# Optimization experiments

Measured on AMD Instinct MI355X. Metric: run time of the kernel, lower is better.

## Reference

```python
import jax, jax.numpy as jnp
import numpy as np

D_MODEL = 1024
N_HEADS = 16
D_K = 64
CHUNK_LEN = 64


def setup_inputs() -> dict:
    key = jax.random.key(0)
    ks = jax.random.split(key, 10)
    B, S = 4, 2048
    NC, NN, NL = 32, 2, 128
    s = 1.0 / np.sqrt(D_MODEL)
    inp = {
        "query": jax.random.normal(ks[0], (B, S, D_MODEL), dtype=jnp.float32),
        "key": jax.random.normal(ks[1], (B, NC, NN, NL, D_MODEL), dtype=jnp.float32),
        # Linear weights stored as [in, out] (equivalent to torch W.T)
        "Wq": jax.random.normal(ks[2], (D_MODEL, N_HEADS * D_K), dtype=jnp.float32) * s,
        "bq": jnp.zeros((N_HEADS * D_K,), dtype=jnp.float32),
        "Wk": jax.random.normal(ks[3], (D_MODEL, N_HEADS * D_K), dtype=jnp.float32) * s,
        "bk": jnp.zeros((N_HEADS * D_K,), dtype=jnp.float32),
        "Wv": jax.random.normal(ks[4], (D_MODEL, N_HEADS * D_K), dtype=jnp.float32) * s,
        "bv": jnp.zeros((N_HEADS * D_K,), dtype=jnp.float32),
        "Wo": jax.random.normal(ks[5], (N_HEADS * D_K, D_MODEL), dtype=jnp.float32) * s,
        "bo": jnp.zeros((D_MODEL,), dtype=jnp.float32),
    }
    return inp


def reference(query, key, Wq, bq, Wk, bk, Wv, bv, Wo, bo):
    B, S, D = query.shape
    _, NC, NN, NL, _ = key.shape
    L = NN * NL  # kv length per chunk
    # reshape query into chunks: [B, NC, chunk_len, D]
    q_in = query.reshape(B, NC, CHUNK_LEN, D)
    kv_in = key.reshape(B, NC, L, D)  # key used for both K and V in the original
    # projections, split heads: [B, NC, H, T, d_k]
    q = (q_in @ Wq + bq).reshape(B, NC, CHUNK_LEN, N_HEADS, D_K).transpose(0, 1, 3, 2, 4)
    k = (kv_in @ Wk + bk).reshape(B, NC, L, N_HEADS, D_K).transpose(0, 1, 3, 2, 4)
    v = (kv_in @ Wv + bv).reshape(B, NC, L, N_HEADS, D_K).transpose(0, 1, 3, 2, 4)
    # attention per (batch, chunk, head)
    scores = jnp.einsum("bchqd,bchkd->bchqk", q, k) / jnp.sqrt(jnp.float32(D_K))
    attn = jax.nn.softmax(scores, axis=-1)
    o = jnp.einsum("bchqk,bchkd->bchqd", attn, v)
    # merge heads: [B, NC, chunk_len, H*d_k]
    o = o.transpose(0, 1, 3, 2, 4).reshape(B, NC, CHUNK_LEN, N_HEADS * D_K)
    out = o @ Wo + bo
    return out.reshape(B, S, D)
```

## Files before the change

### kernel.cpp

```cpp
#include <hip/hip_runtime.h>
#include <hip/hip_bf16.h>
#include <stdint.h>

#define DMODEL 1024
#define NHEADS 16
#define DK 64
#define TQ 64
#define LKV 256
#define MQ 8192
#define MKV 32768

typedef __bf16 bf16x8 __attribute__((ext_vector_type(8)));
typedef float f32x4 __attribute__((ext_vector_type(4)));
typedef unsigned short u16x8 __attribute__((ext_vector_type(8)));

__device__ __forceinline__ unsigned short f2bf(float f) {
    union { float f; unsigned int i; } x; x.f = f;
    unsigned int r = (x.i + 0x7FFFu + ((x.i >> 16) & 1u)) >> 16;
    return (unsigned short)r;
}

__device__ __forceinline__ void gload_lds16(const void* g, void* l) {
    __builtin_amdgcn_global_load_lds(
        (const __attribute__((address_space(1))) unsigned int*)g,
        (__attribute__((address_space(3))) unsigned int*)l, 16, 0, 0);
}

__global__ __launch_bounds__(256) void cvt_f32_bf16(const float* __restrict__ in,
                                                    unsigned short* __restrict__ out) {
    long long i = ((long long)blockIdx.x * 256 + threadIdx.x) * 8;
    f32x4 a = *(const f32x4*)(in + i);
    f32x4 b = *(const f32x4*)(in + i + 4);
    u16x8 o;
    o[0] = f2bf(a[0]); o[1] = f2bf(a[1]); o[2] = f2bf(a[2]); o[3] = f2bf(a[3]);
    o[4] = f2bf(b[0]); o[5] = f2bf(b[1]); o[6] = f2bf(b[2]); o[7] = f2bf(b[3]);
    *(u16x8*)(out + i) = o;
}

__global__ __launch_bounds__(256) void transpose_w_cvt(const float* __restrict__ in,
                                                       unsigned short* __restrict__ out) {
    __shared__ float tile[64][65];
    int bi = blockIdx.y, bj = blockIdx.x;
    int tid = threadIdx.x;
    int c = tid & 63, r0 = tid >> 6;
#pragma unroll
    for (int p = 0; p < 16; ++p) {
        int r = r0 + 4 * p;
        tile[r][c] = in[(size_t)(bi * 64 + r) * 1024 + bj * 64 + c];
    }
    __syncthreads();
#pragma unroll
    for (int p = 0; p < 16; ++p) {
        int r = r0 + 4 * p;
        out[(size_t)(bj * 64 + r) * 1024 + bi * 64 + c] = f2bf(tile[c][r]);
    }
}

template <int OUTMODE>
__global__ __launch_bounds__(256) void gemm_bias(const unsigned short* __restrict__ A,
                                                 const unsigned short* __restrict__ Bt,
                                                 const float* __restrict__ bias,
                                                 void* __restrict__ OutV) {
    __shared__ alignas(16) unsigned short aLds[128 * 32];
    __shared__ alignas(16) unsigned short bLds[128 * 32];

    int tid = threadIdx.x;
    int lane = tid & 63, wid = tid >> 6;
    int m0 = blockIdx.x * 128;
    int n0 = blockIdx.y * 128;
    int wr = (wid >> 1) * 64, wc = (wid & 1) * 64;

    f32x4 zero = {0.f, 0.f, 0.f, 0.f};
    f32x4 acc[4][4];
#pragma unroll
    for (int i = 0; i < 4; ++i)
#pragma unroll
        for (int j = 0; j < 4; ++j) acc[i][j] = zero;

    int sr = lane >> 2;
    int sk = (lane & 3) * 8;
    const unsigned short* aG = A + (size_t)(m0 + sr) * 1024 + sk;
    const unsigned short* bG = Bt + (size_t)(n0 + sr) * 1024 + sk;
    int c0 = wid, c1 = wid + 4;

    int fr = lane & 15, fg = (lane >> 4) * 8;

    for (int kt = 0; kt < 1024; kt += 32) {
        gload_lds16(aG + (size_t)(c0 * 16) * 1024 + kt, aLds + c0 * 512);
        gload_lds16(aG + (size_t)(c1 * 16) * 1024 + kt, aLds + c1 * 512);
        gload_lds16(bG + (size_t)(c0 * 16) * 1024 + kt, bLds + c0 * 512);
        gload_lds16(bG + (size_t)(c1 * 16) * 1024 + kt, bLds + c1 * 512);
        __syncthreads();

        bf16x8 af[4], bf[4];
#pragma unroll
        for (int mt = 0; mt < 4; ++mt)
            af[mt] = *(const bf16x8*)&aLds[(wr + mt * 16 + fr) * 32 + fg];
#pragma unroll
        for (int nt = 0; nt < 4; ++nt)
            bf[nt] = *(const bf16x8*)&bLds[(wc + nt * 16 + fr) * 32 + fg];
#pragma unroll
        for (int mt = 0; mt < 4; ++mt)
#pragma unroll
            for (int nt = 0; nt < 4; ++nt)
                acc[mt][nt] = __builtin_amdgcn_mfma_f32_16x16x32_bf16(af[mt], bf[nt], acc[mt][nt], 0, 0, 0);
        __syncthreads();
    }

    float bv[4];
#pragma unroll
    for (int nt = 0; nt < 4; ++nt) bv[nt] = bias[n0 + wc + nt * 16 + fr];

    if (OUTMODE == 0) {
        unsigned short* Out = (unsigned short*)OutV;
#pragma unroll
        for (int mt = 0; mt < 4; ++mt)
#pragma unroll
            for (int r = 0; r < 4; ++r) {
                size_t row = (size_t)(m0 + wr + mt * 16 + (lane >> 4) * 4 + r);
#pragma unroll
                for (int nt = 0; nt < 4; ++nt)
                    Out[row * 1024 + n0 + wc + nt * 16 + fr] = f2bf(acc[mt][nt][r] + bv[nt]);
            }
    } else if (OUTMODE == 1) {
        unsigned short* Out = (unsigned short*)OutV;
#pragma unroll
        for (int mt = 0; mt < 4; ++mt)
#pragma unroll
            for (int r = 0; r < 4; ++r) {
                int gm = m0 + wr + mt * 16 + (lane >> 4) * 4 + r;
                int bc2 = gm >> 8, lv = gm & 255;
#pragma unroll
                for (int nt = 0; nt < 4; ++nt) {
                    int n = n0 + wc + nt * 16 + fr;
                    int hh = n >> 6, dd = n & 63;
                    Out[(size_t)((bc2 * 16 + hh) * 64 + dd) * 256 + lv] = f2bf(acc[mt][nt][r] + bv[nt]);
                }
            }
    } else {
        float* Out = (float*)OutV;
#pragma unroll
        for (int mt = 0; mt < 4; ++mt)
#pragma unroll
            for (int r = 0; r < 4; ++r) {
                size_t row = (size_t)(m0 + wr + mt * 16 + (lane >> 4) * 4 + r);
#pragma unroll
                for (int nt = 0; nt < 4; ++nt)
                    Out[row * 1024 + n0 + wc + nt * 16 + fr] = acc[mt][nt][r] + bv[nt];
            }
    }
}

__global__ __launch_bounds__(256) void attn_kernel(const unsigned short* __restrict__ Q,
                                                   const unsigned short* __restrict__ K,
                                                   const unsigned short* __restrict__ Vt,
                                                   unsigned short* O) {
    __shared__ alignas(16) unsigned short pLds[64 * 264];

    int tid = threadIdx.x;
    int lane = tid & 63, w = tid >> 6;
    int bc = blockIdx.x >> 4, h = blockIdx.x & 15;
    int fr = lane & 15, g = lane >> 4;

    const unsigned short* qb = Q + (size_t)(bc * 64 + w * 16 + fr) * 1024 + h * 64 + g * 8;
    bf16x8 qf0 = *(const bf16x8*)qb;
    bf16x8 qf1 = *(const bf16x8*)(qb + 32);

    const unsigned short* kb = K + (size_t)(bc * 256 + fr) * 1024 + h * 64 + g * 8;

    f32x4 zero = {0.f, 0.f, 0.f, 0.f};
    f32x4 sc[16];
#pragma unroll
    for (int nt = 0; nt < 16; ++nt) sc[nt] = zero;

#pragma unroll
    for (int nt = 0; nt < 16; ++nt) {
        bf16x8 kf0 = *(const bf16x8*)(kb + (size_t)(nt * 16) * 1024);
        bf16x8 kf1 = *(const bf16x8*)(kb + (size_t)(nt * 16) * 1024 + 32);
        sc[nt] = __builtin_amdgcn_mfma_f32_16x16x32_bf16(qf0, kf0, sc[nt], 0, 0, 0);
        sc[nt] = __builtin_amdgcn_mfma_f32_16x16x32_bf16(qf1, kf1, sc[nt], 0, 0, 0);
    }

    const float scale = 0.125f;
    float mx[4], sum[4];
#pragma unroll
    for (int r = 0; r < 4; ++r) {
        float m = -1e30f;
#pragma unroll
        for (int nt = 0; nt < 16; ++nt) {
            sc[nt][r] *= scale;
            m = fmaxf(m, sc[nt][r]);
        }
#pragma unroll
        for (int x = 1; x < 16; x <<= 1) m = fmaxf(m, __shfl_xor(m, x, 64));
        mx[r] = m;
        sum[r] = 0.f;
    }
#pragma unroll
    for (int nt = 0; nt < 16; ++nt)
#pragma unroll
        for (int r = 0; r < 4; ++r) {
            float p = __expf(sc[nt][r] - mx[r]);
            sum[r] += p;
            pLds[(w * 16 + g * 4 + r) * 264 + nt * 16 + fr] = f2bf(p);
        }
#pragma unroll
    for (int r = 0; r < 4; ++r)
#pragma unroll
        for (int x = 1; x < 16; x <<= 1) sum[r] += __shfl_xor(sum[r], x, 64);

    __syncthreads();

    f32x4 oa[4];
#pragma unroll
    for (int nt = 0; nt < 4; ++nt) oa[nt] = zero;

    const unsigned short* vtb = Vt + (size_t)((bc * 16 + h) * 64) * 256;
#pragma unroll
    for (int ks = 0; ks < 8; ++ks) {
        bf16x8 pf = *(const bf16x8*)&pLds[(w * 16 + fr) * 264 + ks * 32 + g * 8];
#pragma unroll
        for (int nt = 0; nt < 4; ++nt) {
            bf16x8 vf = *(const bf16x8*)(vtb + (size_t)(nt * 16 + fr) * 256 + ks * 32 + g * 8);
            oa[nt] = __builtin_amdgcn_mfma_f32_16x16x32_bf16(pf, vf, oa[nt], 0, 0, 0);
        }
    }

    float rs[4];
#pragma unroll
    for (int r = 0; r < 4; ++r) rs[r] = 1.0f / sum[r];

    unsigned short* ob = O + (size_t)(bc * 64 + w * 16 + g * 4) * 1024 + h * 64 + fr;
#pragma unroll
    for (int nt = 0; nt < 4; ++nt)
#pragma unroll
        for (int r = 0; r < 4; ++r)
            ob[(size_t)r * 1024 + nt * 16] = f2bf(oa[nt][r] * rs[r]);
}

extern "C" void kernel_launch(void* const* d_in, const int* in_sizes, int n_in,
                              void* d_out, int out_size, void* d_ws, size_t ws_size,
                              hipStream_t stream) {
    const float* query = (const float*)d_in[0];
    const float* keyin = (const float*)d_in[1];
    const float* Wq = (const float*)d_in[2];
    const float* bq = (const float*)d_in[3];
    const float* Wk = (const float*)d_in[4];
    const float* bk = (const float*)d_in[5];
    const float* Wv = (const float*)d_in[6];
    const float* bv = (const float*)d_in[7];
    const float* Wo = (const float*)d_in[8];
    const float* bo = (const float*)d_in[9];

    unsigned short* ws = (unsigned short*)d_ws;
    const size_t MB1 = 1024 * 1024;

    unsigned short* WqT = ws;
    unsigned short* WkT = ws + MB1;
    unsigned short* WvT = ws + 2 * MB1;
    unsigned short* WoT = ws + 3 * MB1;
    unsigned short* qb16 = ws + 4 * MB1;
    unsigned short* Qp   = qb16 + (size_t)MQ * 1024;
    unsigned short* kvb  = Qp + (size_t)MQ * 1024;

    size_t ws_elems = ws_size / 2;
    size_t fixed = 4 * MB1 + 2 * (size_t)MQ * 1024;
    size_t avail = (ws_elems > fixed) ? (ws_elems - fixed) : 0;
    long long max_rows = (long long)(avail / (3 * 1024));
    int slice_rows = (int)((max_rows / 256) * 256);
    if (slice_rows > MKV) slice_rows = MKV;
    if (slice_rows < 256) slice_rows = 256;

    unsigned short* Kp = kvb + (size_t)slice_rows * 1024;
    unsigned short* Vt = Kp + (size_t)slice_rows * 1024;

    dim3 tb(256);
    transpose_w_cvt<<<dim3(16, 16), tb, 0, stream>>>(Wq, WqT);
    transpose_w_cvt<<<dim3(16, 16), tb, 0, stream>>>(Wk, WkT);
    transpose_w_cvt<<<dim3(16, 16), tb, 0, stream>>>(Wv, WvT);
    transpose_w_cvt<<<dim3(16, 16), tb, 0, stream>>>(Wo, WoT);

    cvt_f32_bf16<<<dim3(MQ * 1024 / (256 * 8)), tb, 0, stream>>>(query, qb16);
    gemm_bias<0><<<dim3(MQ / 128, 8), tb, 0, stream>>>(qb16, WqT, bq, Qp);

    for (int r0 = 0; r0 < MKV; r0 += slice_rows) {
        int rows = MKV - r0;
        if (rows > slice_rows) rows = slice_rows;
        cvt_f32_bf16<<<dim3(rows * 1024 / (256 * 8)), tb, 0, stream>>>(
            keyin + (size_t)r0 * 1024, kvb);
        gemm_bias<0><<<dim3(rows / 128, 8), tb, 0, stream>>>(kvb, WkT, bk, Kp);
        gemm_bias<1><<<dim3(rows / 128, 8), tb, 0, stream>>>(kvb, WvT, bv, Vt);
        size_t qoff = (size_t)(r0 / 4) * 1024;
        attn_kernel<<<dim3((rows / 256) * 16), tb, 0, stream>>>(
            Qp + qoff, Kp, Vt, Qp + qoff);
    }

    gemm_bias<2><<<dim3(MQ / 128, 8), tb, 0, stream>>>(Qp, WoT, bo, d_out);
}
```

Before: 367.7 us.

## Replace 128x128 GEMM with double-buffered 256x256 tile kernel using swizzled LDS

```diff
diff --git a/kernel.cpp b/kernel.cpp
--- a/kernel.cpp
+++ b/kernel.cpp
@@ -13,6 +13,7 @@
 typedef __bf16 bf16x8 __attribute__((ext_vector_type(8)));
 typedef float f32x4 __attribute__((ext_vector_type(4)));
 typedef unsigned short u16x8 __attribute__((ext_vector_type(8)));
+typedef unsigned short u16;
 
 __device__ __forceinline__ unsigned short f2bf(float f) {
     union { float f; unsigned int i; } x; x.f = f;
@@ -56,97 +57,164 @@
     }
 }
 
+
+__device__ __forceinline__ void stageA64(const u16* src, u16* ldsTile, int row0, int tid) {
+    int w = tid >> 6, l = tid & 63;
+    int r = row0 + w * 8 + (l >> 3);
+    int k16 = (l & 7) ^ ((l >> 3) & 7);
+    gload_lds16(src + (size_t)r * 1024 + k16 * 8, ldsTile + (size_t)(row0 + w * 8) * 64);
+}
+__device__ __forceinline__ void stageB64(const u16* src, u16* ldsTile, int j, int odd, int tid) {
+    int w = tid >> 6, l = tid & 63;
+    int ib = j * 64 + w * 8;
+    int rowbase = ((ib >> 5) << 6) + (ib & 31) + (odd ? 32 : 0);
+    int r = rowbase + (l >> 3);
+    int k16 = (l & 7) ^ ((l >> 3) & 7);
+    gload_lds16(src + (size_t)r * 1024 + k16 * 8, ldsTile + (size_t)rowbase * 64);
+}
+
+#define VMWAIT2() asm volatile("s_waitcnt vmcnt(2)" ::: "memory")
+
 template <int OUTMODE>
-__global__ __launch_bounds__(256) void gemm_bias(const unsigned short* __restrict__ A,
-                                                 const unsigned short* __restrict__ Bt,
-                                                 const float* __restrict__ bias,
-                                                 void* __restrict__ OutV) {
-    __shared__ alignas(16) unsigned short aLds[128 * 32];
-    __shared__ alignas(16) unsigned short bLds[128 * 32];
-
-    int tid = threadIdx.x;
-    int lane = tid & 63, wid = tid >> 6;
-    int m0 = blockIdx.x * 128;
-    int n0 = blockIdx.y * 128;
-    int wr = (wid >> 1) * 64, wc = (wid & 1) * 64;
+__global__ __launch_bounds__(512, 2) void gemm256(const u16* __restrict__ A,
+                                                  const u16* __restrict__ Bt,
+                                                  const float* __restrict__ bias,
+                                                  void* __restrict__ OutV, int nBx) {
+    __shared__ alignas(16) u16 lds[65536];
+    u16* ldsA0 = lds;          u16* ldsA1 = lds + 16384;
+    u16* ldsB0 = lds + 32768;  u16* ldsB1 = lds + 49152;
+
+    int tid = threadIdx.x, lane = tid & 63, wid = tid >> 6;
+    int wm = wid >> 2, wn = wid & 3;
+
+    int nB = nBx * 4;
+    int bid = blockIdx.x;
+    int qq = nB >> 3, rr = nB & 7;
+    int xcd = bid & 7, idx = bid >> 3;
+    int wg = (xcd < rr) ? xcd * (qq + 1) + idx : rr * (qq + 1) + (xcd - rr) * qq + idx;
+    int m0 = (wg >> 2) * 256;
+    int n0 = (wg & 3) * 256;
+
+    const u16* aSrc = A + (size_t)m0 * 1024;
+    const u16* bSrc = Bt + (size_t)n0 * 1024;
 
     f32x4 zero = {0.f, 0.f, 0.f, 0.f};
-    f32x4 acc[4][4];
-#pragma unroll
-    for (int i = 0; i < 4; ++i)
+    f32x4 acc[8][4];
+#pragma unroll
+    for (int i = 0; i < 8; ++i)
 #pragma unroll
         for (int j = 0; j < 4; ++j) acc[i][j] = zero;
 
-    int sr = lane >> 2;
-    int sk = (lane & 3) * 8;
-    const unsigned short* aG = A + (size_t)(m0 + sr) * 1024 + sk;
-    const unsigned short* bG = Bt + (size_t)(n0 + sr) * 1024 + sk;
-    int c0 = wid, c1 = wid + 4;
-
-    int fr = lane & 15, fg = (lane >> 4) * 8;
-
-    for (int kt = 0; kt < 1024; kt += 32) {
-        gload_lds16(aG + (size_t)(c0 * 16) * 1024 + kt, aLds + c0 * 512);
-        gload_lds16(aG + (size_t)(c1 * 16) * 1024 + kt, aLds + c1 * 512);
-        gload_lds16(bG + (size_t)(c0 * 16) * 1024 + kt, bLds + c0 * 512);
-        gload_lds16(bG + (size_t)(c1 * 16) * 1024 + kt, bLds + c1 * 512);
-        __syncthreads();
-
-        bf16x8 af[4], bf[4];
-#pragma unroll
-        for (int mt = 0; mt < 4; ++mt)
-            af[mt] = *(const bf16x8*)&aLds[(wr + mt * 16 + fr) * 32 + fg];
-#pragma unroll
-        for (int nt = 0; nt < 4; ++nt)
-            bf[nt] = *(const bf16x8*)&bLds[(wc + nt * 16 + fr) * 32 + fg];
-#pragma unroll
-        for (int mt = 0; mt < 4; ++mt)
-#pragma unroll
-            for (int nt = 0; nt < 4; ++nt)
-                acc[mt][nt] = __builtin_amdgcn_mfma_f32_16x16x32_bf16(af[mt], bf[nt], acc[mt][nt], 0, 0, 0);
-        __syncthreads();
+    stageA64(aSrc, ldsA0, 0, tid);   stageA64(aSrc, ldsA0, 128, tid);
+    stageB64(bSrc, ldsB0, 0, 0, tid); stageB64(bSrc, ldsB0, 1, 0, tid);
+    stageB64(bSrc, ldsB0, 0, 1, tid); stageB64(bSrc, ldsB0, 1, 1, tid);
+    stageA64(aSrc, ldsA0, 64, tid);  stageA64(aSrc, ldsA0, 192, tid);
+    asm volatile("s_waitcnt vmcnt(0)" ::: "memory");
+    __builtin_amdgcn_s_barrier();
+    asm volatile("" ::: "memory");
+
+    for (int t = 0; t < 16; ++t) {
+        int cur = t & 1;
+        u16* lA = cur ? ldsA1 : ldsA0;
+        u16* lB = cur ? ldsB1 : ldsB0;
+        u16* pA = cur ? ldsA0 : ldsA1;
+        u16* pB = cur ? ldsB0 : ldsB1;
+        const u16* aNext = aSrc + (t + 1) * 64;
+        const u16* bNext = bSrc + (t + 1) * 64;
+        bool pf = (t < 15);
+
+#pragma unroll
+        for (int q = 0; q < 4; ++q) {
+            if (q < 3) VMWAIT2();
+            bf16x8 aF[4][2], bF[2][2];
+            int mrow0 = wm * 128 + (q >> 1) * 64;
+#pragma unroll
+            for (int mf = 0; mf < 4; ++mf) {
+                int row = mrow0 + mf * 16 + (lane & 15);
+#pragma unroll
+                for (int kk = 0; kk < 2; ++kk) {
+                    int k16 = kk * 4 + (lane >> 4);
+                    aF[mf][kk] = *(const bf16x8*)&lA[row * 64 + ((k16 ^ (row & 7)) << 3)];
+                }
+            }
+            int nrow0 = wn * 64 + (q & 1) * 32;
+#pragma unroll
+            for (int nf = 0; nf < 2; ++nf) {
+                int row = nrow0 + nf * 16 + (lane & 15);
+#pragma unroll
+                for (int kk = 0; kk < 2; ++kk) {
+                    int k16 = kk * 4 + (lane >> 4);
+                    bF[nf][kk] = *(const bf16x8*)&lB[row * 64 + ((k16 ^ (row & 7)) << 3)];
+                }
+            }
+            if (pf) {
+                if (q == 0)      { stageA64(aNext, pA, 0, tid);    stageA64(aNext, pA, 128, tid); }
+                else if (q == 1) { stageB64(bNext, pB, 0, 0, tid); stageB64(bNext, pB, 1, 0, tid); }
+                else if (q == 2) { stageB64(bNext, pB, 0, 1, tid); stageB64(bNext, pB, 1, 1, tid); }
+                else             { stageA64(aNext, pA, 64, tid);   stageA64(aNext, pA, 192, tid); }
+            }
+            __builtin_amdgcn_s_barrier();
+            asm volatile("" ::: "memory");
+            __builtin_amdgcn_s_setprio(1);
+#pragma unroll
+            for (int mf = 0; mf < 4; ++mf)
+#pragma unroll
+                for (int nf = 0; nf < 2; ++nf)
+#pragma unroll
+                    for (int kk = 0; kk < 2; ++kk)
+                        acc[(q >> 1) * 4 + mf][(q & 1) * 2 + nf] =
+                            __builtin_amdgcn_mfma_f32_16x16x32_bf16(
+                                aF[mf][kk], bF[nf][kk],
+                                acc[(q >> 1) * 4 + mf][(q & 1) * 2 + nf], 0, 0, 0);
+            __builtin_amdgcn_s_setprio(0);
+            __builtin_amdgcn_s_barrier();
+            asm volatile("" ::: "memory");
+        }
     }
 
     float bv[4];
 #pragma unroll
-    for (int nt = 0; nt < 4; ++nt) bv[nt] = bias[n0 + wc + nt * 16 + fr];
+    for (int NF = 0; NF < 4; ++NF) bv[NF] = bias[n0 + wn * 64 + NF * 16 + (lane & 15)];
 
     if (OUTMODE == 0) {
-        unsigned short* Out = (unsigned short*)OutV;
-#pragma unroll
-        for (int mt = 0; mt < 4; ++mt)
+        u16* Out = (u16*)OutV;
+#pragma unroll
+        for (int MF = 0; MF < 8; ++MF)
 #pragma unroll
             for (int r = 0; r < 4; ++r) {
-                size_t row = (size_t)(m0 + wr + mt * 16 + (lane >> 4) * 4 + r);
-#pragma unroll
-                for (int nt = 0; nt < 4; ++nt)
-                    Out[row * 1024 + n0 + wc + nt * 16 + fr] = f2bf(acc[mt][nt][r] + bv[nt]);
+                size_t row = (size_t)(m0 + wm * 128 + MF * 16 + (lane >> 4) * 4 + r);
+#pragma unroll
+                for (int NF = 0; NF < 4; ++NF)
+                    Out[row * 1024 + n0 + wn * 64 + NF * 16 + (lane & 15)] =
+                        f2bf(acc[MF][NF][r] + bv[NF]);
             }
     } else if (OUTMODE == 1) {
-        unsigned short* Out = (unsigned short*)OutV;
-#pragma unroll
-        for (int mt = 0; mt < 4; ++mt)
+        u16* Out = (u16*)OutV;
+#pragma unroll
+        for (int MF = 0; MF < 8; ++MF)
 #pragma unroll
             for (int r = 0; r < 4; ++r) {
-                int gm = m0 + wr + mt * 16 + (lane >> 4) * 4 + r;
+                int gm = m0 + wm * 128 + MF * 16 + (lane >> 4) * 4 + r;
                 int bc2 = gm >> 8, lv = gm & 255;
 #pragma unroll
-                for (int nt = 0; nt < 4; ++nt) {
-                    int n = n0 + wc + nt * 16 + fr;
+                for (int NF = 0; NF < 4; ++NF) {
+                    int n = n0 + wn * 64 + NF * 16 + (lane & 15);
                     int hh = n >> 6, dd = n & 63;
-                    Out[(size_t)((bc2 * 16 + hh) * 64 + dd) * 256 + lv] = f2bf(acc[mt][nt][r] + bv[nt]);
+                    Out[(size_t)((bc2 * 16 + hh) * 64 + dd) * 256 + lv] =
+                        f2bf(acc[MF][NF][r] + bv[NF]);
                 }
             }
     } else {
         float* Out = (float*)OutV;
 #pragma unroll
-        for (int mt = 0; mt < 4; ++mt)
+        for (int MF = 0; MF < 8; ++MF)
 #pragma unroll
             for (int r = 0; r < 4; ++r) {
-                size_t row = (size_t)(m0 + wr + mt * 16 + (lane >> 4) * 4 + r);
-#pragma unroll
-                for (int nt = 0; nt < 4; ++nt)
-                    Out[row * 1024 + n0 + wc + nt * 16 + fr] = acc[mt][nt][r] + bv[nt];
+                size_t row = (size_t)(m0 + wm * 128 + MF * 16 + (lane >> 4) * 4 + r);
+#pragma unroll
+                for (int NF = 0; NF < 4; ++NF)
+                    Out[row * 1024 + n0 + wn * 64 + NF * 16 + (lane & 15)] =
+                        acc[MF][NF][r] + bv[NF];
             }
     }
 }
@@ -281,19 +349,19 @@
     transpose_w_cvt<<<dim3(16, 16), tb, 0, stream>>>(Wo, WoT);
 
     cvt_f32_bf16<<<dim3(MQ * 1024 / (256 * 8)), tb, 0, stream>>>(query, qb16);
-    gemm_bias<0><<<dim3(MQ / 128, 8), tb, 0, stream>>>(qb16, WqT, bq, Qp);
+    gemm256<0><<<dim3((MQ / 256) * 4), dim3(512), 0, stream>>>(qb16, WqT, bq, Qp, MQ / 256);
 
     for (int r0 = 0; r0 < MKV; r0 += slice_rows) {
         int rows = MKV - r0;
         if (rows > slice_rows) rows = slice_rows;
         cvt_f32_bf16<<<dim3(rows * 1024 / (256 * 8)), tb, 0, stream>>>(
             keyin + (size_t)r0 * 1024, kvb);
-        gemm_bias<0><<<dim3(rows / 128, 8), tb, 0, stream>>>(kvb, WkT, bk, Kp);
-        gemm_bias<1><<<dim3(rows / 128, 8), tb, 0, stream>>>(kvb, WvT, bv, Vt);
+        gemm256<0><<<dim3((rows / 256) * 4), dim3(512), 0, stream>>>(kvb, WkT, bk, Kp, rows / 256);
+        gemm256<1><<<dim3((rows / 256) * 4), dim3(512), 0, stream>>>(kvb, WvT, bv, Vt, rows / 256);
         size_t qoff = (size_t)(r0 / 4) * 1024;
         attn_kernel<<<dim3((rows / 256) * 16), tb, 0, stream>>>(
             Qp + qoff, Kp, Vt, Qp + qoff);
     }
 
-    gemm_bias<2><<<dim3(MQ / 128, 8), tb, 0, stream>>>(Qp, WoT, bo, d_out);
-}
+    gemm256<2><<<dim3((MQ / 256) * 4), dim3(512), 0, stream>>>(Qp, WoT, bo, d_out, MQ / 256);
+}
```

Result: no change. 363.9 us (-1.0%).
